# Kernel optimization log

Hardware: AMD Instinct MI355X
Metric: run time of the kernel (lower is better)

## Reference

```python
import jax, jax.numpy as jnp
import numpy as np

MUL = 32          # channel multiplicity of node features (32x0e + 32x1o)
N_SPEC = 4        # one-hot species dim (node_attrs = 4x0e)
N_EMB = 8         # radial (bessel) embedding dim
HID = 8           # invariant_neurons
TP_W = 4 * MUL    # tp.weight_numel: 4 'uvu' paths, 32 weights each
INV_SQRT3 = 0.5773502691896258


def setup_inputs() -> dict:
    key = jax.random.key(0)
    ks = jax.random.split(key, 13)
    N, E = 50000, 800000
    node_features = jax.random.normal(ks[0], (N, 4 * MUL), jnp.float32)
    node_attrs = jax.random.uniform(ks[1], (N, N_SPEC), dtype=jnp.float32)
    edge_index = jax.random.randint(ks[2], (2, E), 0, N)
    edge_attrs = jax.random.normal(ks[3], (E, 4), jnp.float32)          # SH: [0e | 1o(3)]
    edge_embedding = jax.random.uniform(ks[4], (E, N_EMB), dtype=jnp.float32)
    # learned parameters
    W1_s = jax.random.normal(ks[5], (MUL, MUL), jnp.float32)            # linear_1 scalar block
    W1_v = jax.random.normal(ks[6], (MUL, MUL), jnp.float32)            # linear_1 vector block
    fc_w1 = jax.random.normal(ks[7], (N_EMB, HID), jnp.float32)         # radial MLP layer 1
    fc_w2 = jax.random.normal(ks[8], (HID, TP_W), jnp.float32)          # radial MLP -> tp weights
    W2_s = jax.random.normal(ks[9], (2 * MUL, MUL), jnp.float32)        # linear_2: 64x0e -> 32x0e
    W2_v = jax.random.normal(ks[10], (2 * MUL, MUL), jnp.float32)       # linear_2: 64x1o -> 32x1o
    Wsc_s = jax.random.normal(ks[11], (MUL, N_SPEC, MUL), jnp.float32)  # sc: 0e x 0e -> 0e (uvw)
    Wsc_v = jax.random.normal(ks[12], (MUL, N_SPEC, MUL), jnp.float32)  # sc: 1o x 0e -> 1o (uvw)
    return dict(node_features=node_features, node_attrs=node_attrs,
                edge_attrs=edge_attrs, edge_embedding=edge_embedding,
                W1_s=W1_s, W1_v=W1_v, fc_w1=fc_w1, fc_w2=fc_w2,
                W2_s=W2_s, W2_v=W2_v, Wsc_s=Wsc_s, Wsc_v=Wsc_v,
                edge_index=edge_index)


def reference(node_features, node_attrs, edge_attrs, edge_embedding,
              W1_s, W1_v, fc_w1, fc_w2, W2_s, W2_v, Wsc_s, Wsc_v, edge_index):
    N = node_features.shape[0]
    edge_src = edge_index[1]
    edge_dst = edge_index[0]

    # split node features into scalar (32x0e) and vector (32x1o) blocks
    s = node_features[:, :MUL]                       # [N, 32]
    v = node_features[:, MUL:].reshape(N, MUL, 3)    # [N, 32, 3]

    # --- self-connection: FullyConnectedTensorProduct(features, node_attrs) ---
    sc_norm = 1.0 / jnp.sqrt(jnp.float32(MUL * N_SPEC))
    sc_s = jnp.einsum('nu,na,uaw->nw', s, node_attrs, Wsc_s) * sc_norm
    sc_v = jnp.einsum('nui,na,uaw->nwi', v, node_attrs, Wsc_v) * sc_norm

    # --- linear_1 (per-irrep linear, fan-in normalized) ---
    l1 = 1.0 / jnp.sqrt(jnp.float32(MUL))
    s1 = (s @ W1_s) * l1                                   # [N, 32]
    v1 = jnp.einsum('nui,uw->nwi', v, W1_v) * l1           # [N, 32, 3]

    # --- radial MLP: edge_embedding -> per-edge tp weights (silu) ---
    h = jax.nn.silu((edge_embedding @ fc_w1) / jnp.sqrt(jnp.float32(N_EMB)))
    w = (h @ fc_w2) / jnp.sqrt(jnp.float32(HID))           # [E, 128]
    w0, w1, w2, w3 = w[:, :MUL], w[:, MUL:2*MUL], w[:, 2*MUL:3*MUL], w[:, 3*MUL:]

    # --- gather source-node features per edge ---
    ss = s1[edge_src]                                      # [E, 32]
    vv = v1[edge_src]                                      # [E, 32, 3]
    a0 = edge_attrs[:, 0]                                  # [E]    0e SH
    a1 = edge_attrs[:, 1:4]                                # [E, 3] 1o SH

    # --- 'uvu' CG tensor product (4 paths) with per-edge weights ---
    o_s0 = w0 * ss * a0[:, None]                                    # 0e x 0e -> 0e
    o_s1 = w3 * jnp.einsum('eui,ei->eu', vv, a1) * INV_SQRT3        # 1o x 1o -> 0e
    o_v0 = w1[:, :, None] * ss[:, :, None] * a1[:, None, :]        # 0e x 1o -> 1o
    o_v1 = w2[:, :, None] * vv * a0[:, None, None]                 # 1o x 0e -> 1o

    eS = jnp.concatenate([o_s0, o_s1], axis=1)             # [E, 64] (64x0e)
    eV = jnp.concatenate([o_v0, o_v1], axis=1)             # [E, 64, 3] (64x1o)

    # --- scatter-add to destination nodes ---
    S = jax.ops.segment_sum(eS, edge_dst, num_segments=N)  # [N, 64]
    V = jax.ops.segment_sum(eV, edge_dst, num_segments=N)  # [N, 64, 3]

    # --- linear_2 (64x0e+64x1o -> 32x0e+32x1o) ---
    l2 = 1.0 / jnp.sqrt(jnp.float32(2 * MUL))
    s_out = (S @ W2_s) * l2
    v_out = jnp.einsum('nui,uw->nwi', V, W2_v) * l2

    # --- residual self-connection ---
    s_out = s_out + sc_s
    v_out = v_out + sc_v
    return jnp.concatenate([s_out, v_out.reshape(N, MUL * 3)], axis=1)  # [N, 128]
```

## Files before the change

### kernel.cpp

```cpp
#include <hip/hip_runtime.h>
#include <math.h>


typedef float  v2f __attribute__((ext_vector_type(2)));
typedef float  v4f __attribute__((ext_vector_type(4)));

__device__ __forceinline__ unsigned short f2bf(float x) {
    unsigned u = __float_as_uint(x);
    u += 0x7FFFu + ((u >> 16) & 1u);
    return (unsigned short)(u >> 16);
}
__device__ __forceinline__ float bf2f(unsigned short h) {
    return __uint_as_float(((unsigned)h) << 16);
}
__device__ __forceinline__ unsigned pack_bf(float lo, float hi) {
    unsigned ul = __float_as_uint(lo);
    ul = (ul + (0x7FFFu + ((ul >> 16) & 1u))) >> 16;
    unsigned uh = __float_as_uint(hi);
    uh = (uh + (0x7FFFu + ((uh >> 16) & 1u))) & 0xFFFF0000u;
    return ul | uh;
}
__device__ __forceinline__ float bf_lo(unsigned p) { return __uint_as_float(p << 16); }
__device__ __forceinline__ float bf_hi(unsigned p) { return __uint_as_float(p & 0xFFFF0000u); }

__global__ __launch_bounds__(256) void node_prep(
    const float* __restrict__ nf, const float* __restrict__ W1_s,
    const float* __restrict__ W1_v, const int* __restrict__ eidx,
    int* __restrict__ cnt, ushort* __restrict__ sv1, int N, int E)
{
    __shared__ float w1s[1024];
    __shared__ float w1v[1024];
    __shared__ float nrow[8][128];

    for (long long e = (long long)blockIdx.x * 256 + threadIdx.x; e < E;
         e += (long long)gridDim.x * 256)
        atomicAdd(cnt + eidx[(int)e], 1);

    int g = threadIdx.x >> 5;
    int w = threadIdx.x & 31;
    int n = blockIdx.x * 8 + g;

    for (int i = threadIdx.x; i < 1024; i += 256) {
        w1s[i] = W1_s[i];
        w1v[i] = W1_v[i];
    }
    if (n < N) {
        float4 q = *(const float4*)(nf + (size_t)n * 128 + w * 4);
        *(float4*)&nrow[g][w * 4] = q;
    }
    __syncthreads();
    if (n >= N) return;

    const float l1 = 0.17677669529663687f;
    const float* r = nrow[g];
    float ss = 0.f, vx = 0.f, vy = 0.f, vz = 0.f;
#pragma unroll 8
    for (int u = 0; u < 32; ++u) {
        float ws = w1s[u * 32 + w];
        float wv = w1v[u * 32 + w];
        ss += r[u] * ws;
        vx += r[32 + u * 3 + 0] * wv;
        vy += r[32 + u * 3 + 1] * wv;
        vz += r[32 + u * 3 + 2] * wv;
    }
    ushort4 o;
    o.x = f2bf(ss * l1); o.y = f2bf(vx * l1);
    o.z = f2bf(vy * l1); o.w = f2bf(vz * l1);
    *(ushort4*)(sv1 + (size_t)n * 128 + w * 4) = o;
}


__global__ __launch_bounds__(1024) void scan_a(
    const int* __restrict__ cnt, int* __restrict__ rs,
    int* __restrict__ bsum, int N)
{
    int i = blockIdx.x * 1024 + threadIdx.x;
    int lane = threadIdx.x & 63;
    int wid = threadIdx.x >> 6;
    int v = (i < N) ? cnt[i] : 0;
    int incl = v;
#pragma unroll
    for (int d = 1; d < 64; d <<= 1) {
        int t = __shfl_up(incl, d);
        if (lane >= d) incl += t;
    }
    __shared__ int wtot[16];
    __shared__ int woff[16];
    if (lane == 63) wtot[wid] = incl;
    __syncthreads();
    if (wid == 0) {
        int t = (lane < 16) ? wtot[lane] : 0;
        int s = t;
#pragma unroll
        for (int d = 1; d < 16; d <<= 1) {
            int q = __shfl_up(s, d);
            if (lane >= d) s += q;
        }
        if (lane < 16) woff[lane] = s - t;
        if (lane == 15) bsum[blockIdx.x] = s;
    }
    __syncthreads();
    if (i < N) rs[i] = woff[wid] + incl - v;
}

__global__ __launch_bounds__(64) void scan_b(
    const int* __restrict__ bsum, int* __restrict__ boff, int nb)
{
    int lane = threadIdx.x;
    int carry = 0;
    for (int base = 0; base < nb; base += 64) {
        int i = base + lane;
        int v = (i < nb) ? bsum[i] : 0;
        int s = v;
#pragma unroll
        for (int d = 1; d < 64; d <<= 1) {
            int t = __shfl_up(s, d);
            if (lane >= d) s += t;
        }
        if (i < nb) boff[i] = carry + s - v;
        carry += __shfl(s, 63);
    }
}

__global__ __launch_bounds__(256) void scatter_build(
    const float* __restrict__ ea, const float* __restrict__ ee,
    const float* __restrict__ fc1, const int* __restrict__ eidx,
    int* __restrict__ rs, const int* __restrict__ boff,
    unsigned* __restrict__ recb, int E)
{
    int e = blockIdx.x * 256 + threadIdx.x;
    if (e >= E) return;
    const float rs8 = 0.35355339059327373f;

    int d = eidx[e];
    int src = eidx[E + e];
    int p = atomicAdd(rs + d, 1) + boff[d >> 10];

    const float* eep = ee + (size_t)e * 8;
    v4f e0 = *(const v4f*)eep;
    v4f e1 = *(const v4f*)(eep + 4);
    float ev[8] = {e0.x, e0.y, e0.z, e0.w, e1.x, e1.y, e1.z, e1.w};
    float hh[8];
#pragma unroll
    for (int k = 0; k < 8; ++k) {
        float t = 0.f;
#pragma unroll
        for (int i = 0; i < 8; ++i) t += ev[i] * fc1[i * 8 + k];
        t *= rs8;
        hh[k] = t * __builtin_amdgcn_rcpf(1.f + __expf(-t)) * rs8;
    }
    uint4 hp;
    hp.x = pack_bf(hh[0], hh[1]);
    hp.y = pack_bf(hh[2], hh[3]);
    hp.z = pack_bf(hh[4], hh[5]);
    hp.w = pack_bf(hh[6], hh[7]);
    v4f a = *(const v4f*)(ea + (size_t)e * 4);
    uint4 t2;
    t2.x = pack_bf(a.x, a.y);
    t2.y = pack_bf(a.z, a.w);
    t2.z = (unsigned)src;
    t2.w = 0u;
    unsigned* rp = recb + (size_t)p * 8;
    *(uint4*)rp       = hp;
    *(uint4*)(rp + 4) = t2;
}


__global__ __launch_bounds__(64) void reduce_kernel(
    const float* __restrict__ fc2, const ushort* __restrict__ sv1,
    const unsigned* __restrict__ recb, const int* __restrict__ rs_end,
    const int* __restrict__ boff, const int* __restrict__ cnt,
    ushort* __restrict__ SVb, int N)
{
    __shared__ float rec[64][20];

    int l = threadIdx.x;
    int h = l >> 5;
    int u = l & 31;
    int n = blockIdx.x;

    const float inv_sqrt3 = 0.5773502691896258f;

    v2f f01[8], f23[8];
#pragma unroll
    for (int k = 0; k < 8; ++k) {
        f01[k].x = fc2[k * 128 + u];
        f01[k].y = fc2[k * 128 + 32 + u];
        f23[k].x = fc2[k * 128 + 64 + u];
        f23[k].y = fc2[k * 128 + 96 + u];
    }

    int count = cnt[n];
    int start = rs_end[n] + boff[n >> 10] - count;

    float aS0 = 0.f, aS1 = 0.f;
    float aV0x = 0.f, aV0y = 0.f, aV0z = 0.f;
    float aV1x = 0.f, aV1y = 0.f, aV1z = 0.f;

    for (int j0 = 0; j0 < count; j0 += 64) {
        int nk = count - j0; if (nk > 64) nk = 64;
        if (l < nk) {
            const unsigned* rp = recb + (size_t)(start + j0 + l) * 8;
            uint4 hq = *(const uint4*)rp;
            uint4 aq = *(const uint4*)(rp + 4);
            float* rr = &rec[l][0];
            *(v4f*)rr       = (v4f){bf_lo(hq.x), bf_hi(hq.x), bf_lo(hq.y), bf_hi(hq.y)};
            *(v4f*)(rr + 4) = (v4f){bf_lo(hq.z), bf_hi(hq.z), bf_lo(hq.w), bf_hi(hq.w)};
            *(v4f*)(rr + 8) = (v4f){bf_lo(aq.x), bf_hi(aq.x), bf_lo(aq.y), bf_hi(aq.y)};
            rr[12] = __uint_as_float(aq.z);
        }
        int pairs = (nk + 1) >> 1;
        int last = nk - 1;
        int s0 = __float_as_int(rec[h <= last ? h : last][12]);
        ushort4 q = *(const ushort4*)(sv1 + (size_t)s0 * 128 + u * 4);
        for (int jj = 0; jj < pairs; ++jj) {
            int slot = jj * 2 + h;
            int nslot = slot + 2 <= last ? slot + 2 : last;
            int sN = __float_as_int(rec[nslot][12]);
            ushort4 qn = *(const ushort4*)(sv1 + (size_t)sN * 128 + u * 4);

            float msk = (slot <= last) ? 1.f : 0.f;
            int slotc = slot <= last ? slot : last;
            const float* rr = &rec[slotc][0];
            v4f H0 = *(const v4f*)rr;
            v4f H1 = *(const v4f*)(rr + 4);
            v4f A  = *(const v4f*)(rr + 8);
            float ss = bf2f(q.x) * msk;
            float vx = bf2f(q.y), vy = bf2f(q.z), vz = bf2f(q.w);

            v2f w01 = H0.x * f01[0] + H0.y * f01[1] + H0.z * f01[2] + H0.w * f01[3]
                    + H1.x * f01[4] + H1.y * f01[5] + H1.z * f01[6] + H1.w * f01[7];
            v2f w23 = H0.x * f23[0] + H0.y * f23[1] + H0.z * f23[2] + H0.w * f23[3]
                    + H1.x * f23[4] + H1.y * f23[5] + H1.z * f23[6] + H1.w * f23[7];

            float dv = (vx * A.y + vy * A.z + vz * A.w) * msk;
            aS0 += w01.x * (ss * A.x);
            aS1 += w23.y * dv;
            float c1 = w01.y * ss;
            aV0x += c1 * A.y; aV0y += c1 * A.z; aV0z += c1 * A.w;
            float c2 = w23.x * A.x * msk;
            aV1x += c2 * vx; aV1y += c2 * vy; aV1z += c2 * vz;
            q = qn;
        }
    }

    aS0  += __shfl_xor(aS0, 32);
    aS1  += __shfl_xor(aS1, 32);
    aV0x += __shfl_xor(aV0x, 32);
    aV0y += __shfl_xor(aV0y, 32);
    aV0z += __shfl_xor(aV0z, 32);
    aV1x += __shfl_xor(aV1x, 32);
    aV1y += __shfl_xor(aV1y, 32);
    aV1z += __shfl_xor(aV1z, 32);

    if (h == 0) {
        uint4 o;
        o.x = pack_bf(aS0, aS1 * inv_sqrt3);
        o.y = pack_bf(aV0x, aV0y);
        o.z = pack_bf(aV0z, aV1x);
        o.w = pack_bf(aV1y, aV1z);
        *(uint4*)(SVb + (size_t)n * 256 + u * 8) = o;
    }
}


__global__ __launch_bounds__(256) void node_final(
    const ushort* __restrict__ SVb, const float* __restrict__ W2_s,
    const float* __restrict__ W2_v, const float* __restrict__ nf,
    const float* __restrict__ nattr, const float* __restrict__ Wsc_s,
    const float* __restrict__ Wsc_v, float* __restrict__ out, int N)
{
    __shared__ uint2 wqb[1024];
    __shared__ uint2 wsv_s[1024];
    __shared__ uint2 wsv_v[1024];
    __shared__ v2f   svtp[8][32][5];
    __shared__ float nrow[8][128];

    int g = threadIdx.x >> 5;
    int w = threadIdx.x & 31;

    for (int i = threadIdx.x; i < 1024; i += 256) {
        int uu = i >> 5, ww = i & 31;
        wqb[i] = (uint2){pack_bf(W2_s[i], W2_v[i]),
                         pack_bf(W2_s[i + 1024], W2_v[i + 1024])};
        const float* ps = Wsc_s + (size_t)uu * 128 + ww;
        const float* pv = Wsc_v + (size_t)uu * 128 + ww;
        wsv_s[i] = (uint2){pack_bf(ps[0], ps[32]), pack_bf(ps[64], ps[96])};
        wsv_v[i] = (uint2){pack_bf(pv[0], pv[32]), pack_bf(pv[64], pv[96])};
    }
    __syncthreads();

    const float l2 = 0.125f;
    const float sc_norm = 0.08838834764831843f;

    for (int t = 0; t < 2; ++t) {
        int n = blockIdx.x * 16 + g * 2 + t;
        if (n >= N) continue;
        uint4 p = *(const uint4*)(SVb + (size_t)n * 256 + w * 8);
        svtp[g][w][0] = (v2f){bf_lo(p.x), bf_lo(p.z)};
        svtp[g][w][1] = (v2f){bf_hi(p.x), bf_hi(p.w)};
        svtp[g][w][2] = (v2f){bf_lo(p.y), bf_hi(p.y)};
        svtp[g][w][3] = (v2f){bf_hi(p.z), bf_lo(p.w)};
        float4 q = *(const float4*)(nf + (size_t)n * 128 + w * 4);
        *(float4*)&nrow[g][w * 4] = q;
        float at0 = nattr[(size_t)n * 4 + 0];
        float at1 = nattr[(size_t)n * 4 + 1];
        float at2 = nattr[(size_t)n * 4 + 2];
        float at3 = nattr[(size_t)n * 4 + 3];

        v2f sa_va2 = (v2f){0.f, 0.f};
        v2f va01   = (v2f){0.f, 0.f};
        v2f scv01  = (v2f){0.f, 0.f};
        float scs = 0.f, scv2 = 0.f;
#pragma unroll
        for (int u = 0; u < 32; ++u) {
            int idx = u * 32 + w;
            uint2 qw = wqb[idx];
            float w2s_a = bf_lo(qw.x), w2v_a = bf_hi(qw.x);
            float w2s_b = bf_lo(qw.y), w2v_b = bf_hi(qw.y);
            v2f Q0 = svtp[g][u][0], Q1 = svtp[g][u][1];
            v2f Q2 = svtp[g][u][2], Q3 = svtp[g][u][3];
            sa_va2 += Q0 * (v2f){w2s_a, w2v_a};
            sa_va2 += Q1 * (v2f){w2s_b, w2v_b};
            va01   += Q2 * (v2f){w2v_a, w2v_a};
            va01   += Q3 * (v2f){w2v_b, w2v_b};
            uint2 wsq = wsv_s[idx];
            uint2 wvq = wsv_v[idx];
            v2f csv = at0 * (v2f){bf_lo(wsq.x), bf_lo(wvq.x)}
                    + at1 * (v2f){bf_hi(wsq.x), bf_hi(wvq.x)}
                    + at2 * (v2f){bf_lo(wsq.y), bf_lo(wvq.y)}
                    + at3 * (v2f){bf_hi(wsq.y), bf_hi(wvq.y)};
            float su = nrow[g][u];
            float vx = nrow[g][32 + u * 3 + 0];
            float vy = nrow[g][32 + u * 3 + 1];
            float vz = nrow[g][32 + u * 3 + 2];
            scs   += su * csv.x;
            scv01 += (v2f){vx, vy} * (v2f){csv.y, csv.y};
            scv2  += vz * csv.y;
        }
        float* orow = out + (size_t)n * 128;
        orow[w]              = sa_va2.x * l2 + scs     * sc_norm;
        orow[32 + w * 3 + 0] = va01.x   * l2 + scv01.x * sc_norm;
        orow[32 + w * 3 + 1] = va01.y   * l2 + scv01.y * sc_norm;
        orow[32 + w * 3 + 2] = sa_va2.y * l2 + scv2    * sc_norm;
    }
}


__global__ __launch_bounds__(256) void edge_kernel(
    const float* __restrict__ ea, const float* __restrict__ ee,
    const float* __restrict__ fc1, const float* __restrict__ fc2,
    const ushort* __restrict__ sv1, const int* __restrict__ eidx,
    float* __restrict__ SV, int E)
{
    long long tid = (long long)blockIdx.x * 256 + threadIdx.x;
    int e = (int)(tid >> 5);
    int u = (int)(tid & 31);
    if (e >= E) return;
    const float rs8 = 0.35355339059327373f;
    const float inv_sqrt3 = 0.5773502691896258f;
    float ev[8];
#pragma unroll
    for (int i = 0; i < 8; ++i) ev[i] = ee[(size_t)e * 8 + i];
    float h[8];
#pragma unroll
    for (int k = 0; k < 8; ++k) {
        float t = 0.f;
#pragma unroll
        for (int i = 0; i < 8; ++i) t += ev[i] * fc1[i * 8 + k];
        t *= rs8;
        h[k] = t / (1.f + expf(-t));
    }
    float w0 = 0.f, w1 = 0.f, w2 = 0.f, w3 = 0.f;
#pragma unroll
    for (int k = 0; k < 8; ++k) {
        const float* f2 = fc2 + k * 128;
        float hk = h[k];
        w0 += hk * f2[u];
        w1 += hk * f2[32 + u];
        w2 += hk * f2[64 + u];
        w3 += hk * f2[96 + u];
    }
    w0 *= rs8; w1 *= rs8; w2 *= rs8; w3 *= rs8;
    int dst = eidx[e];
    int src = eidx[E + e];
    float a0 = ea[(size_t)e * 4 + 0];
    float ax = ea[(size_t)e * 4 + 1];
    float ay = ea[(size_t)e * 4 + 2];
    float az = ea[(size_t)e * 4 + 3];
    ushort4 q = *(const ushort4*)(sv1 + (size_t)src * 128 + u * 4);
    float ss = bf2f(q.x), vx = bf2f(q.y), vy = bf2f(q.z), vz = bf2f(q.w);
    float dv = vx * ax + vy * ay + vz * az;
    float* o = SV + (size_t)dst * 256 + u * 8;
    atomicAdd(o + 0, w0 * ss * a0);
    atomicAdd(o + 1, w3 * dv * inv_sqrt3);
    float c1 = w1 * ss;
    atomicAdd(o + 2, c1 * ax);
    atomicAdd(o + 3, c1 * ay);
    atomicAdd(o + 4, c1 * az);
    float c2 = w2 * a0;
    atomicAdd(o + 5, c2 * vx);
    atomicAdd(o + 6, c2 * vy);
    atomicAdd(o + 7, c2 * vz);
}

__global__ __launch_bounds__(256) void node_final_f32(
    const float* __restrict__ SV, const float* __restrict__ W2_s,
    const float* __restrict__ W2_v, const float* __restrict__ nf,
    const float* __restrict__ nattr, const float* __restrict__ Wsc_s,
    const float* __restrict__ Wsc_v, float* __restrict__ out, int N)
{
    __shared__ float wq[4096];
    __shared__ float wsp[4096];
    __shared__ float wvp[4096];
    __shared__ float svt[8][8][32];
    __shared__ float nrow[8][128];

    int g = threadIdx.x >> 5;
    int w = threadIdx.x & 31;

    for (int i = threadIdx.x; i < 1024; i += 256) {
        int uu = i >> 5, ww = i & 31;
        *(float4*)&wq[i * 4] = make_float4(W2_s[i], W2_s[i + 1024],
                                           W2_v[i], W2_v[i + 1024]);
        const float* ps = Wsc_s + (size_t)uu * 128 + ww;
        const float* pv = Wsc_v + (size_t)uu * 128 + ww;
        *(float4*)&wsp[i * 4] = make_float4(ps[0], ps[32], ps[64], ps[96]);
        *(float4*)&wvp[i * 4] = make_float4(pv[0], pv[32], pv[64], pv[96]);
    }
    __syncthreads();

    const float l2 = 0.125f;
    const float sc_norm = 0.08838834764831843f;

    for (int t = 0; t < 4; ++t) {
        int n = blockIdx.x * 32 + g * 4 + t;
        if (n >= N) continue;
        const float* svp = SV + (size_t)n * 256 + w * 8;
        float4 p0 = *(const float4*)svp;
        float4 p1 = *(const float4*)(svp + 4);
        svt[g][0][w] = p0.x; svt[g][1][w] = p0.y;
        svt[g][2][w] = p0.z; svt[g][3][w] = p0.w;
        svt[g][4][w] = p1.x; svt[g][5][w] = p1.y;
        svt[g][6][w] = p1.z; svt[g][7][w] = p1.w;
        float4 q = *(const float4*)(nf + (size_t)n * 128 + w * 4);
        *(float4*)&nrow[g][w * 4] = q;
        float at0 = nattr[(size_t)n * 4 + 0];
        float at1 = nattr[(size_t)n * 4 + 1];
        float at2 = nattr[(size_t)n * 4 + 2];
        float at3 = nattr[(size_t)n * 4 + 3];

        float sa = 0.f, va0 = 0.f, va1 = 0.f, va2 = 0.f;
        float scs = 0.f, scv0 = 0.f, scv1 = 0.f, scv2 = 0.f;
#pragma unroll
        for (int u = 0; u < 32; ++u) {
            float4 qw = *(const float4*)&wq[(u * 32 + w) * 4];
            sa  += svt[g][0][u] * qw.x + svt[g][1][u] * qw.y;
            va0 += svt[g][2][u] * qw.z + svt[g][5][u] * qw.w;
            va1 += svt[g][3][u] * qw.z + svt[g][6][u] * qw.w;
            va2 += svt[g][4][u] * qw.z + svt[g][7][u] * qw.w;
            float4 ps = *(const float4*)&wsp[(u * 32 + w) * 4];
            float4 pv = *(const float4*)&wvp[(u * 32 + w) * 4];
            float cs = at0 * ps.x + at1 * ps.y + at2 * ps.z + at3 * ps.w;
            float cv = at0 * pv.x + at1 * pv.y + at2 * pv.z + at3 * pv.w;
            scs  += nrow[g][u] * cs;
            scv0 += nrow[g][32 + u * 3 + 0] * cv;
            scv1 += nrow[g][32 + u * 3 + 1] * cv;
            scv2 += nrow[g][32 + u * 3 + 2] * cv;
        }
        float* orow = out + (size_t)n * 128;
        orow[w] = sa * l2 + scs * sc_norm;
        orow[32 + w * 3 + 0] = va0 * l2 + scv0 * sc_norm;
        orow[32 + w * 3 + 1] = va1 * l2 + scv1 * sc_norm;
        orow[32 + w * 3 + 2] = va2 * l2 + scv2 * sc_norm;
    }
}

extern "C" void kernel_launch(void* const* d_in, const int* in_sizes, int n_in,
                              void* d_out, int out_size, void* d_ws, size_t ws_size,
                              hipStream_t stream) {
    const float* nf    = (const float*)d_in[0];
    const float* nattr = (const float*)d_in[1];
    const float* ea    = (const float*)d_in[2];
    const float* ee    = (const float*)d_in[3];
    const float* W1_s  = (const float*)d_in[4];
    const float* W1_v  = (const float*)d_in[5];
    const float* fc1   = (const float*)d_in[6];
    const float* fc2   = (const float*)d_in[7];
    const float* W2_s  = (const float*)d_in[8];
    const float* W2_v  = (const float*)d_in[9];
    const float* Wsc_s = (const float*)d_in[10];
    const float* Wsc_v = (const float*)d_in[11];
    const int*   eidx  = (const int*)d_in[12];

    int N = in_sizes[0] / 128;
    int E = in_sizes[12] / 2;

    float* ws = (float*)d_ws;
    ushort* sv1 = (ushort*)ws;
    ushort* SVb = (ushort*)(ws + (size_t)N * 64);
    unsigned* recb = (unsigned*)(ws + (size_t)N * 192);
    int* cnt  = (int*)(ws + (size_t)N * 192 + (size_t)E * 8);
    int* rs   = cnt + N;
    int* bsum = rs + N;
    int* boff = bsum + 64;

    size_t needed = ((size_t)N * 194 + (size_t)E * 8 + 128) * 4;

    int nb_node = (N + 7) / 8;
    int nbE = (E + 255) / 256;

    if (ws_size >= needed) {
        hipMemsetAsync(cnt, 0, (size_t)N * sizeof(int), stream);
        node_prep<<<nb_node, 256, 0, stream>>>(nf, W1_s, W1_v, eidx, cnt, sv1, N, E);
        int nbS = (N + 1023) / 1024;
        scan_a<<<nbS, 1024, 0, stream>>>(cnt, rs, bsum, N);
        scan_b<<<1, 64, 0, stream>>>(bsum, boff, nbS);
        scatter_build<<<nbE, 256, 0, stream>>>(ea, ee, fc1, eidx, rs, boff,
                                               recb, E);
        reduce_kernel<<<N, 64, 0, stream>>>(fc2, sv1, recb, rs, boff, cnt,
                                            SVb, N);
        int nb_final = (N + 15) / 16;
        node_final<<<nb_final, 256, 0, stream>>>(SVb, W2_s, W2_v, nf, nattr,
                                                 Wsc_s, Wsc_v, (float*)d_out, N);
    } else {
        float* SVf = ws + (size_t)N * 64;
        int* cnt_f = (int*)(SVf + (size_t)N * 256);
        hipMemsetAsync(SVf, 0, (size_t)N * 256 * sizeof(float), stream);
        node_prep<<<nb_node, 256, 0, stream>>>(nf, W1_s, W1_v, eidx, cnt_f, sv1, N, E);
        long long tot = (long long)E * 32;
        int nb_edge = (int)((tot + 255) / 256);
        edge_kernel<<<nb_edge, 256, 0, stream>>>(ea, ee, fc1, fc2, sv1, eidx, SVf, E);
        int nb_final_f = (N + 31) / 32;
        node_final_f32<<<nb_final_f, 256, 0, stream>>>(SVf, W2_s, W2_v, nf, nattr,
                                                       Wsc_s, Wsc_v, (float*)d_out, N);
    }
}
```

Baseline: 218.2 us.

## Move self-connection into node_prep and slim node_final to linear_2 only

The residual self-connection (Wsc contracted with node attributes and node features) is now computed in node_prep, which already loads each node row, and written straight to the output. node_final then only does linear_2 on the reduced edge sums and adds its result into the output, so it no longer reloads node features, attributes or the Wsc tables. node_final also processes its two nodes with shared weight loads in one loop. The trade is that node_prep gets heavier (more shared memory and math), and node_final now does a read-modify-write of the output instead of a plain store.

```diff
diff --git a/kernel.cpp b/kernel.cpp
--- a/kernel.cpp
+++ b/kernel.cpp
@@ -25,11 +25,17 @@
 
 __global__ __launch_bounds__(256) void node_prep(
     const float* __restrict__ nf, const float* __restrict__ W1_s,
-    const float* __restrict__ W1_v, const int* __restrict__ eidx,
-    int* __restrict__ cnt, ushort* __restrict__ sv1, int N, int E)
+    const float* __restrict__ W1_v, const float* __restrict__ nattr,
+    const float* __restrict__ Wsc_s, const float* __restrict__ Wsc_v,
+    const int* __restrict__ eidx, int* __restrict__ cnt,
+    ushort* __restrict__ sv1, float* __restrict__ out, int N, int E)
 {
     __shared__ float w1s[1024];
     __shared__ float w1v[1024];
+    __shared__ v2f ws_s01[1024];
+    __shared__ v2f ws_s23[1024];
+    __shared__ v2f ws_v01[1024];
+    __shared__ v2f ws_v23[1024];
     __shared__ float nrow[8][128];
 
     for (long long e = (long long)blockIdx.x * 256 + threadIdx.x; e < E;
@@ -43,6 +49,13 @@
     for (int i = threadIdx.x; i < 1024; i += 256) {
         w1s[i] = W1_s[i];
         w1v[i] = W1_v[i];
+        int uu = i >> 5, ww = i & 31;
+        const float* ps = Wsc_s + (size_t)uu * 128 + ww;
+        const float* pv = Wsc_v + (size_t)uu * 128 + ww;
+        ws_s01[i] = (v2f){ps[0],  ps[32]};
+        ws_s23[i] = (v2f){ps[64], ps[96]};
+        ws_v01[i] = (v2f){pv[0],  pv[32]};
+        ws_v23[i] = (v2f){pv[64], pv[96]};
     }
     if (n < N) {
         float4 q = *(const float4*)(nf + (size_t)n * 128 + w * 4);
@@ -52,21 +65,44 @@
     if (n >= N) return;
 
     const float l1 = 0.17677669529663687f;
+    const float sc_norm = 0.08838834764831843f;
+    v2f at01 = (v2f){nattr[(size_t)n * 4 + 0], nattr[(size_t)n * 4 + 1]};
+    v2f at23 = (v2f){nattr[(size_t)n * 4 + 2], nattr[(size_t)n * 4 + 3]};
+
     const float* r = nrow[g];
     float ss = 0.f, vx = 0.f, vy = 0.f, vz = 0.f;
+    float scs = 0.f, scv0 = 0.f, scv1 = 0.f, scv2 = 0.f;
 #pragma unroll 8
     for (int u = 0; u < 32; ++u) {
-        float ws = w1s[u * 32 + w];
-        float wv = w1v[u * 32 + w];
-        ss += r[u] * ws;
-        vx += r[32 + u * 3 + 0] * wv;
-        vy += r[32 + u * 3 + 1] * wv;
-        vz += r[32 + u * 3 + 2] * wv;
+        int idx = u * 32 + w;
+        float ru = r[u];
+        float rx = r[32 + u * 3 + 0];
+        float ry = r[32 + u * 3 + 1];
+        float rz = r[32 + u * 3 + 2];
+        float wsv = w1v[idx];
+        ss += ru * w1s[idx];
+        vx += rx * wsv;
+        vy += ry * wsv;
+        vz += rz * wsv;
+        v2f ts = at01 * ws_s01[idx] + at23 * ws_s23[idx];
+        v2f tv = at01 * ws_v01[idx] + at23 * ws_v23[idx];
+        float cs = ts.x + ts.y;
+        float cv = tv.x + tv.y;
+        scs  += ru * cs;
+        scv0 += rx * cv;
+        scv1 += ry * cv;
+        scv2 += rz * cv;
     }
     ushort4 o;
     o.x = f2bf(ss * l1); o.y = f2bf(vx * l1);
     o.z = f2bf(vy * l1); o.w = f2bf(vz * l1);
     *(ushort4*)(sv1 + (size_t)n * 128 + w * 4) = o;
+
+    float* orow = out + (size_t)n * 128;
+    orow[w]              = scs  * sc_norm;
+    orow[32 + w * 3 + 0] = scv0 * sc_norm;
+    orow[32 + w * 3 + 1] = scv1 * sc_norm;
+    orow[32 + w * 3 + 2] = scv2 * sc_norm;
 }
 
 
@@ -266,83 +302,71 @@
 
 __global__ __launch_bounds__(256) void node_final(
     const ushort* __restrict__ SVb, const float* __restrict__ W2_s,
-    const float* __restrict__ W2_v, const float* __restrict__ nf,
-    const float* __restrict__ nattr, const float* __restrict__ Wsc_s,
-    const float* __restrict__ Wsc_v, float* __restrict__ out, int N)
+    const float* __restrict__ W2_v, float* __restrict__ out, int N)
 {
     __shared__ uint2 wqb[1024];
-    __shared__ uint2 wsv_s[1024];
-    __shared__ uint2 wsv_v[1024];
-    __shared__ v2f   svtp[8][32][5];
-    __shared__ float nrow[8][128];
+    __shared__ v2f   svtp[8][2][32][5];
 
     int g = threadIdx.x >> 5;
     int w = threadIdx.x & 31;
 
-    for (int i = threadIdx.x; i < 1024; i += 256) {
-        int uu = i >> 5, ww = i & 31;
+    for (int i = threadIdx.x; i < 1024; i += 256)
         wqb[i] = (uint2){pack_bf(W2_s[i], W2_v[i]),
                          pack_bf(W2_s[i + 1024], W2_v[i + 1024])};
-        const float* ps = Wsc_s + (size_t)uu * 128 + ww;
-        const float* pv = Wsc_v + (size_t)uu * 128 + ww;
-        wsv_s[i] = (uint2){pack_bf(ps[0], ps[32]), pack_bf(ps[64], ps[96])};
-        wsv_v[i] = (uint2){pack_bf(pv[0], pv[32]), pack_bf(pv[64], pv[96])};
-    }
     __syncthreads();
 
     const float l2 = 0.125f;
-    const float sc_norm = 0.08838834764831843f;
-
-    for (int t = 0; t < 2; ++t) {
-        int n = blockIdx.x * 16 + g * 2 + t;
-        if (n >= N) continue;
-        uint4 p = *(const uint4*)(SVb + (size_t)n * 256 + w * 8);
-        svtp[g][w][0] = (v2f){bf_lo(p.x), bf_lo(p.z)};
-        svtp[g][w][1] = (v2f){bf_hi(p.x), bf_hi(p.w)};
-        svtp[g][w][2] = (v2f){bf_lo(p.y), bf_hi(p.y)};
-        svtp[g][w][3] = (v2f){bf_hi(p.z), bf_lo(p.w)};
-        float4 q = *(const float4*)(nf + (size_t)n * 128 + w * 4);
-        *(float4*)&nrow[g][w * 4] = q;
-        float at0 = nattr[(size_t)n * 4 + 0];
-        float at1 = nattr[(size_t)n * 4 + 1];
-        float at2 = nattr[(size_t)n * 4 + 2];
-        float at3 = nattr[(size_t)n * 4 + 3];
-
-        v2f sa_va2 = (v2f){0.f, 0.f};
-        v2f va01   = (v2f){0.f, 0.f};
-        v2f scv01  = (v2f){0.f, 0.f};
-        float scs = 0.f, scv2 = 0.f;
-#pragma unroll
-        for (int u = 0; u < 32; ++u) {
-            int idx = u * 32 + w;
-            uint2 qw = wqb[idx];
-            float w2s_a = bf_lo(qw.x), w2v_a = bf_hi(qw.x);
-            float w2s_b = bf_lo(qw.y), w2v_b = bf_hi(qw.y);
-            v2f Q0 = svtp[g][u][0], Q1 = svtp[g][u][1];
-            v2f Q2 = svtp[g][u][2], Q3 = svtp[g][u][3];
-            sa_va2 += Q0 * (v2f){w2s_a, w2v_a};
-            sa_va2 += Q1 * (v2f){w2s_b, w2v_b};
-            va01   += Q2 * (v2f){w2v_a, w2v_a};
-            va01   += Q3 * (v2f){w2v_b, w2v_b};
-            uint2 wsq = wsv_s[idx];
-            uint2 wvq = wsv_v[idx];
-            v2f csv = at0 * (v2f){bf_lo(wsq.x), bf_lo(wvq.x)}
-                    + at1 * (v2f){bf_hi(wsq.x), bf_hi(wvq.x)}
-                    + at2 * (v2f){bf_lo(wsq.y), bf_lo(wvq.y)}
-                    + at3 * (v2f){bf_hi(wsq.y), bf_hi(wvq.y)};
-            float su = nrow[g][u];
-            float vx = nrow[g][32 + u * 3 + 0];
-            float vy = nrow[g][32 + u * 3 + 1];
-            float vz = nrow[g][32 + u * 3 + 2];
-            scs   += su * csv.x;
-            scv01 += (v2f){vx, vy} * (v2f){csv.y, csv.y};
-            scv2  += vz * csv.y;
-        }
-        float* orow = out + (size_t)n * 128;
-        orow[w]              = sa_va2.x * l2 + scs     * sc_norm;
-        orow[32 + w * 3 + 0] = va01.x   * l2 + scv01.x * sc_norm;
-        orow[32 + w * 3 + 1] = va01.y   * l2 + scv01.y * sc_norm;
-        orow[32 + w * 3 + 2] = sa_va2.y * l2 + scv2    * sc_norm;
+
+    int n0 = blockIdx.x * 16 + g * 2;
+    int n1 = n0 + 1;
+    if (n0 < N) {
+        uint4 p = *(const uint4*)(SVb + (size_t)n0 * 256 + w * 8);
+        svtp[g][0][w][0] = (v2f){bf_lo(p.x), bf_lo(p.z)};
+        svtp[g][0][w][1] = (v2f){bf_hi(p.x), bf_hi(p.w)};
+        svtp[g][0][w][2] = (v2f){bf_lo(p.y), bf_hi(p.y)};
+        svtp[g][0][w][3] = (v2f){bf_hi(p.z), bf_lo(p.w)};
+    }
+    if (n1 < N) {
+        uint4 p = *(const uint4*)(SVb + (size_t)n1 * 256 + w * 8);
+        svtp[g][1][w][0] = (v2f){bf_lo(p.x), bf_lo(p.z)};
+        svtp[g][1][w][1] = (v2f){bf_hi(p.x), bf_hi(p.w)};
+        svtp[g][1][w][2] = (v2f){bf_lo(p.y), bf_hi(p.y)};
+        svtp[g][1][w][3] = (v2f){bf_hi(p.z), bf_lo(p.w)};
+    }
+
+    v2f sa0 = (v2f){0.f, 0.f}, va0 = (v2f){0.f, 0.f};
+    v2f sa1 = (v2f){0.f, 0.f}, va1 = (v2f){0.f, 0.f};
+#pragma unroll
+    for (int u = 0; u < 32; ++u) {
+        uint2 qw = wqb[u * 32 + w];
+        float w2s_a = bf_lo(qw.x), w2v_a = bf_hi(qw.x);
+        float w2s_b = bf_lo(qw.y), w2v_b = bf_hi(qw.y);
+        v2f wa  = (v2f){w2s_a, w2v_a};
+        v2f wb  = (v2f){w2s_b, w2v_b};
+        v2f wva = (v2f){w2v_a, w2v_a};
+        v2f wvb = (v2f){w2v_b, w2v_b};
+        sa0 += svtp[g][0][u][0] * wa;
+        sa0 += svtp[g][0][u][1] * wb;
+        va0 += svtp[g][0][u][2] * wva;
+        va0 += svtp[g][0][u][3] * wvb;
+        sa1 += svtp[g][1][u][0] * wa;
+        sa1 += svtp[g][1][u][1] * wb;
+        va1 += svtp[g][1][u][2] * wva;
+        va1 += svtp[g][1][u][3] * wvb;
+    }
+    if (n0 < N) {
+        float* orow = out + (size_t)n0 * 128;
+        orow[w]              += sa0.x * l2;
+        orow[32 + w * 3 + 0] += va0.x * l2;
+        orow[32 + w * 3 + 1] += va0.y * l2;
+        orow[32 + w * 3 + 2] += sa0.y * l2;
+    }
+    if (n1 < N) {
+        float* orow = out + (size_t)n1 * 128;
+        orow[w]              += sa1.x * l2;
+        orow[32 + w * 3 + 0] += va1.x * l2;
+        orow[32 + w * 3 + 1] += va1.y * l2;
+        orow[32 + w * 3 + 2] += sa1.y * l2;
     }
 }
 
@@ -406,32 +430,20 @@
 
 __global__ __launch_bounds__(256) void node_final_f32(
     const float* __restrict__ SV, const float* __restrict__ W2_s,
-    const float* __restrict__ W2_v, const float* __restrict__ nf,
-    const float* __restrict__ nattr, const float* __restrict__ Wsc_s,
-    const float* __restrict__ Wsc_v, float* __restrict__ out, int N)
+    const float* __restrict__ W2_v, float* __restrict__ out, int N)
 {
     __shared__ float wq[4096];
-    __shared__ float wsp[4096];
-    __shared__ float wvp[4096];
     __shared__ float svt[8][8][32];
-    __shared__ float nrow[8][128];
 
     int g = threadIdx.x >> 5;
     int w = threadIdx.x & 31;
 
-    for (int i = threadIdx.x; i < 1024; i += 256) {
-        int uu = i >> 5, ww = i & 31;
+    for (int i = threadIdx.x; i < 1024; i += 256)
         *(float4*)&wq[i * 4] = make_float4(W2_s[i], W2_s[i + 1024],
                                            W2_v[i], W2_v[i + 1024]);
-        const float* ps = Wsc_s + (size_t)uu * 128 + ww;
-        const float* pv = Wsc_v + (size_t)uu * 128 + ww;
-        *(float4*)&wsp[i * 4] = make_float4(ps[0], ps[32], ps[64], ps[96]);
-        *(float4*)&wvp[i * 4] = make_float4(pv[0], pv[32], pv[64], pv[96]);
-    }
     __syncthreads();
 
     const float l2 = 0.125f;
-    const float sc_norm = 0.08838834764831843f;
 
     for (int t = 0; t < 4; ++t) {
         int n = blockIdx.x * 32 + g * 4 + t;
@@ -443,15 +455,8 @@
         svt[g][2][w] = p0.z; svt[g][3][w] = p0.w;
         svt[g][4][w] = p1.x; svt[g][5][w] = p1.y;
         svt[g][6][w] = p1.z; svt[g][7][w] = p1.w;
-        float4 q = *(const float4*)(nf + (size_t)n * 128 + w * 4);
-        *(float4*)&nrow[g][w * 4] = q;
-        float at0 = nattr[(size_t)n * 4 + 0];
-        float at1 = nattr[(size_t)n * 4 + 1];
-        float at2 = nattr[(size_t)n * 4 + 2];
-        float at3 = nattr[(size_t)n * 4 + 3];
 
         float sa = 0.f, va0 = 0.f, va1 = 0.f, va2 = 0.f;
-        float scs = 0.f, scv0 = 0.f, scv1 = 0.f, scv2 = 0.f;
 #pragma unroll
         for (int u = 0; u < 32; ++u) {
             float4 qw = *(const float4*)&wq[(u * 32 + w) * 4];
@@ -459,20 +464,12 @@
             va0 += svt[g][2][u] * qw.z + svt[g][5][u] * qw.w;
             va1 += svt[g][3][u] * qw.z + svt[g][6][u] * qw.w;
             va2 += svt[g][4][u] * qw.z + svt[g][7][u] * qw.w;
-            float4 ps = *(const float4*)&wsp[(u * 32 + w) * 4];
-            float4 pv = *(const float4*)&wvp[(u * 32 + w) * 4];
-            float cs = at0 * ps.x + at1 * ps.y + at2 * ps.z + at3 * ps.w;
-            float cv = at0 * pv.x + at1 * pv.y + at2 * pv.z + at3 * pv.w;
-            scs  += nrow[g][u] * cs;
-            scv0 += nrow[g][32 + u * 3 + 0] * cv;
-            scv1 += nrow[g][32 + u * 3 + 1] * cv;
-            scv2 += nrow[g][32 + u * 3 + 2] * cv;
         }
         float* orow = out + (size_t)n * 128;
-        orow[w] = sa * l2 + scs * sc_norm;
-        orow[32 + w * 3 + 0] = va0 * l2 + scv0 * sc_norm;
-        orow[32 + w * 3 + 1] = va1 * l2 + scv1 * sc_norm;
-        orow[32 + w * 3 + 2] = va2 * l2 + scv2 * sc_norm;
+        orow[w]              += sa  * l2;
+        orow[32 + w * 3 + 0] += va0 * l2;
+        orow[32 + w * 3 + 1] += va1 * l2;
+        orow[32 + w * 3 + 2] += va2 * l2;
     }
 }
 
@@ -512,7 +509,9 @@
 
     if (ws_size >= needed) {
         hipMemsetAsync(cnt, 0, (size_t)N * sizeof(int), stream);
-        node_prep<<<nb_node, 256, 0, stream>>>(nf, W1_s, W1_v, eidx, cnt, sv1, N, E);
+        node_prep<<<nb_node, 256, 0, stream>>>(nf, W1_s, W1_v, nattr, Wsc_s,
+                                               Wsc_v, eidx, cnt, sv1,
+                                               (float*)d_out, N, E);
         int nbS = (N + 1023) / 1024;
         scan_a<<<nbS, 1024, 0, stream>>>(cnt, rs, bsum, N);
         scan_b<<<1, 64, 0, stream>>>(bsum, boff, nbS);
@@ -521,18 +520,21 @@
         reduce_kernel<<<N, 64, 0, stream>>>(fc2, sv1, recb, rs, boff, cnt,
                                             SVb, N);
         int nb_final = (N + 15) / 16;
-        node_final<<<nb_final, 256, 0, stream>>>(SVb, W2_s, W2_v, nf, nattr,
-                                                 Wsc_s, Wsc_v, (float*)d_out, N);
+        node_final<<<nb_final, 256, 0, stream>>>(SVb, W2_s, W2_v,
+                                                 (float*)d_out, N);
     } else {
         float* SVf = ws + (size_t)N * 64;
         int* cnt_f = (int*)(SVf + (size_t)N * 256);
         hipMemsetAsync(SVf, 0, (size_t)N * 256 * sizeof(float), stream);
-        node_prep<<<nb_node, 256, 0, stream>>>(nf, W1_s, W1_v, eidx, cnt_f, sv1, N, E);
+        hipMemsetAsync(cnt_f, 0, (size_t)N * sizeof(int), stream);
+        node_prep<<<nb_node, 256, 0, stream>>>(nf, W1_s, W1_v, nattr, Wsc_s,
+                                               Wsc_v, eidx, cnt_f, sv1,
+                                               (float*)d_out, N, E);
         long long tot = (long long)E * 32;
         int nb_edge = (int)((tot + 255) / 256);
         edge_kernel<<<nb_edge, 256, 0, stream>>>(ea, ee, fc1, fc2, sv1, eidx, SVf, E);
         int nb_final_f = (N + 31) / 32;
-        node_final_f32<<<nb_final_f, 256, 0, stream>>>(SVf, W2_s, W2_v, nf, nattr,
-                                                       Wsc_s, Wsc_v, (float*)d_out, N);
-    }
-}
+        node_final_f32<<<nb_final_f, 256, 0, stream>>>(SVf, W2_s, W2_v,
+                                                       (float*)d_out, N);
+    }
+}
```

Result: slower. 282.7 us (+29.6%).
